# Kernel tuning notes

Hardware: AMD Instinct MI355X
Metric: run time of the kernel (lower is better)

The kernel has to match this reference:

```python
import jax, jax.numpy as jnp
import numpy as np
from jax import lax

DIM = 256
PROJ = 128
NPOS = 8          # ceil(log2(2*64+5))
EXT = 64          # attnExtension
NLAYERS = 4
HEADS = 4
KDIM = PROJ + NPOS
EPS = 1e-5


def _ln(x):
    # LayerNorm over last dim, no affine (elementwise_affine=False)
    mu = jnp.mean(x, axis=-1, keepdims=True)
    var = jnp.mean(jnp.square(x - mu), axis=-1, keepdims=True)
    return (x - mu) * lax.rsqrt(var + EPS)


def setup_inputs() -> dict:
    key = jax.random.key(0)
    ks = jax.random.split(key, 18)
    L = 2048
    s = 0.05
    return {
        "input": jax.random.normal(ks[0], (L, PROJ), jnp.float32),
        "residual": jax.random.normal(ks[1], (5 * L, DIM), jnp.float32),
        "W_proj": jax.random.normal(ks[2], (5 * DIM, KDIM), jnp.float32) * s,
        "b_proj": jnp.zeros((5 * DIM,), jnp.float32),
        "Wq": jax.random.normal(ks[3], (DIM, DIM), jnp.float32) * s,
        "bq": jnp.zeros((DIM,), jnp.float32),
        "Wk": jax.random.normal(ks[4], (DIM, KDIM), jnp.float32) * s,
        "bk": jnp.zeros((DIM,), jnp.float32),
        "Wv": jax.random.normal(ks[5], (DIM, KDIM), jnp.float32) * s,
        "bv": jnp.zeros((DIM,), jnp.float32),
        "Wo": jax.random.normal(ks[6], (DIM, DIM), jnp.float32) * s,
        "bo": jnp.zeros((DIM,), jnp.float32),
        "conv_w": jax.random.normal(ks[7], (NLAYERS, DIM, DIM, 3), jnp.float32) * s,
        "conv_b": jnp.zeros((NLAYERS, DIM), jnp.float32),
        "W_skip": jax.random.normal(ks[8], (DIM, DIM), jnp.float32) * s,
        "b_skip": jnp.zeros((DIM,), jnp.float32),
    }


def reference(input, residual, W_proj, b_proj, Wq, bq, Wk, bk, Wv, bv,
              Wo, bo, conv_w, conv_b, W_skip, b_skip):
    L = input.shape[0]
    T = 5 * L  # tgt length
    hd = DIM // HEADS

    # positional embeddings: pos[:, i] = (arange(L) % 2^(i+1)) / 2^i
    n = jnp.arange(L, dtype=input.dtype)[:, None]
    i = jnp.arange(NPOS, dtype=input.dtype)[None, :]
    pos = jnp.mod(n, 2.0 ** (i + 1.0)) / (2.0 ** i)

    src = jnp.concatenate([input, pos], axis=1)            # (L, KDIM)
    tgt = (src @ W_proj.T + b_proj).reshape(T, DIM)        # (5L, DIM)

    # banded mask: row j may attend col i iff 5i-EXT <= j < 5i+5+EXT
    j = jnp.arange(T)[:, None]
    ii = jnp.arange(L)[None, :]
    d = j - 5 * ii
    allowed = (d >= -EXT) & (d < 5 + EXT)                  # (5L, L)

    # multihead attention (eval mode, dropout skipped)
    q = (tgt @ Wq.T + bq).reshape(T, HEADS, hd).transpose(1, 0, 2)
    k = (src @ Wk.T + bk).reshape(L, HEADS, hd).transpose(1, 0, 2)
    v = (src @ Wv.T + bv).reshape(L, HEADS, hd).transpose(1, 0, 2)
    scores = jnp.einsum('hqd,hkd->hqk', q, k) / jnp.sqrt(jnp.asarray(hd, q.dtype))
    scores = jnp.where(allowed[None], scores, -jnp.inf)
    attn = jax.nn.softmax(scores, axis=-1)
    ctx = jnp.einsum('hqk,hkd->hqd', attn, v).transpose(1, 0, 2).reshape(T, DIM)
    attn_out = ctx @ Wo.T + bo

    cnn_in = _ln(attn_out) + residual                      # (5L, DIM)

    # spectral-norm conv stack (weights assumed pre-normalized) + tanh
    x = cnn_in.T[None]                                     # (1, DIM, 5L)
    for l in range(NLAYERS):
        x = jnp.tanh(
            lax.conv_general_dilated(x, conv_w[l], window_strides=(1,),
                                     padding=[(1, 1)])
            + conv_b[l][None, :, None])
    cnn_out = x[0].T                                       # (5L, DIM)

    return _ln(cnn_out + cnn_in @ W_skip.T + b_skip)
```

## Files before the change

### kernel.cpp

```cpp
#include <hip/hip_runtime.h>
#include <hip/hip_bf16.h>

#define PROJ 128
#define KPAD 192
#define EPS 1e-5f

typedef __attribute__((ext_vector_type(4))) float f32x4;
typedef __attribute__((ext_vector_type(8))) short bf16x8;
typedef __attribute__((ext_vector_type(4))) unsigned int u32x4;

__device__ inline float bflo(unsigned u){ union{unsigned x;float f;}c; c.x = u<<16; return c.f; }
__device__ inline float bfhi(unsigned u){ union{unsigned x;float f;}c; c.x = u & 0xffff0000u; return c.f; }
__device__ inline float bf2f(unsigned short u){ union{unsigned x;float f;}c; c.x = ((unsigned)u)<<16; return c.f; }
__device__ inline unsigned short f2bf(float f){
    union{float f; unsigned u;} c; c.f = f;
    unsigned r = c.u + 0x7fff + ((c.u >> 16) & 1);
    return (unsigned short)(r >> 16);
}
__device__ __forceinline__ bf16x8 asbf(u32x4 u){ union{u32x4 a; bf16x8 b;} c; c.a = u; return c.b; }

__global__ __launch_bounds__(256) void prep_all(
    const float* __restrict__ W_proj, const float* __restrict__ Wq,
    const float* __restrict__ Wk, const float* __restrict__ Wv,
    const float* __restrict__ Wo, const float* __restrict__ Ws,
    const float* __restrict__ convw, const float* __restrict__ input,
    const float* __restrict__ bq, const float* __restrict__ b_proj,
    unsigned short* __restrict__ Wqb, unsigned short* __restrict__ Wkb,
    unsigned short* __restrict__ Wvb, unsigned short* __restrict__ Wob,
    unsigned short* __restrict__ Wsb, unsigned short* __restrict__ Wcb,
    unsigned short* __restrict__ WpbT, unsigned short* __restrict__ srcb,
    unsigned short* __restrict__ cinp, float* __restrict__ zbias,
    float* __restrict__ bqc, int L, int T)
{
    int idx = blockIdx.x * 256 + threadIdx.x;
    if (idx < 65536) { Wqb[idx] = f2bf(Wq[idx]); return; }
    idx -= 65536;
    if (idx < 49152) {
        int r = idx / 192, c = idx % 192;
        Wkb[idx] = (c < 136) ? f2bf(Wk[(size_t)r * 136 + c]) : (unsigned short)0;
        return;
    }
    idx -= 49152;
    if (idx < 49152) {
        int r = idx / 192, c = idx % 192;
        Wvb[idx] = (c < 136) ? f2bf(Wv[(size_t)r * 136 + c]) : (unsigned short)0;
        return;
    }
    idx -= 49152;
    if (idx < 65536) { Wob[idx] = f2bf(Wo[idx]); return; }
    idx -= 65536;
    if (idx < 65536) {
        int e = idx & 7;
        int lane = (idx >> 3) & 63;
        int fr = (idx >> 9) & 3;
        int wid = (idx >> 11) & 7;
        int kt = idx >> 14;
        int j = fr >> 1, ks = fr & 1;
        int kq = lane >> 4, rowf = lane & 15;
        int o = wid * 32 + j * 16 + rowf;
        int c = kt * 64 + ks * 32 + kq * 8 + e;
        Wsb[idx] = f2bf(Ws[(size_t)o * 256 + c]);
        return;
    }
    idx -= 65536;
    if (idx < 786432) {
        int e = idx & 7;
        int lane = (idx >> 3) & 63;
        int fr = (idx >> 9) & 3;
        int wid = (idx >> 11) & 7;
        int ktl = idx >> 14;
        int l = ktl / 12, kt = ktl % 12;
        int j = fr >> 1, ks = fr & 1;
        int kq = lane >> 4, rowf = lane & 15;
        int o = wid * 32 + j * 16 + rowf;
        int c = kt * 64 + ks * 32 + kq * 8 + e;
        int ktap = c >> 8, ci = c & 255;
        Wcb[idx] = f2bf(convw[(((size_t)l * 256 + o) * 256 + ci) * 3 + ktap]);
        return;
    }
    idx -= 786432;
    if (idx < 327680) {
        int r = idx >> 16;
        int rem = idx & 65535;
        int c = rem >> 8, d = rem & 255;
        WpbT[idx] = (c < 136) ? f2bf(W_proj[(size_t)(r * 256 + d) * 136 + c])
                              : (unsigned short)0;
        return;
    }
    idx -= 327680;
    if (idx < L * KPAD) {
        int n = idx / KPAD, c = idx % KPAD;
        float v = 0.f;
        if (c < PROJ) v = input[(size_t)n * PROJ + c];
        else if (c < PROJ + 8) {
            int i = c - PROJ;
            int mask = (2 << i) - 1;
            v = (float)(n & mask) / (float)(1 << i);
        }
        srcb[idx] = f2bf(v);
        return;
    }
    idx -= L * KPAD;
    if (idx < 512) {
        int row = idx >> 8, c = idx & 255;
        size_t o = (row == 0) ? (size_t)c : (size_t)(T + 1) * 256 + c;
        cinp[o] = 0;
        return;
    }
    idx -= 512;
    if (idx < 256) { zbias[idx] = 0.f; return; }
    idx -= 256;
    if (idx < 1280) {
        int r = idx >> 8, o = idx & 255;
        float s = bq[o];
        const float* wrow = Wq + (size_t)o * 256;
        const float* bp = b_proj + r * 256;
        for (int c = 0; c < 256; ++c) s += wrow[c] * bp[c];
        bqc[idx] = s;
    }
}

__device__ __forceinline__ void gemm_core_64x128(
    unsigned short (&As)[64][72], unsigned short (&Bs)[128][72],
    const unsigned short* __restrict__ A, int lda,
    const unsigned short* __restrict__ B, int ldb,
    const float* __restrict__ bias,
    unsigned short* __restrict__ C, int ldc,
    int K, int m0, int n0)
{
    const int tid = threadIdx.x;
    const int lane = tid & 63;
    const int wid = tid >> 6;
    const int wm = wid >> 1, wn = wid & 1;

    const int ar = tid >> 2, asg = tid & 3;
    const int br = tid >> 1, bsg = tid & 1;

    const unsigned short* Ap = A + (size_t)(m0 + ar) * lda + asg * 16;
    const unsigned short* Bp = B + (size_t)(n0 + br) * ldb + bsg * 32;

    u32x4 ra0, ra1, rb0, rb1, rb2, rb3;
    auto loadregs = [&](int k0) {
        ra0 = *(const u32x4*)(Ap + k0);
        ra1 = *(const u32x4*)(Ap + k0 + 8);
        rb0 = *(const u32x4*)(Bp + k0);
        rb1 = *(const u32x4*)(Bp + k0 + 8);
        rb2 = *(const u32x4*)(Bp + k0 + 16);
        rb3 = *(const u32x4*)(Bp + k0 + 24);
    };
    auto stlds = [&]() {
        *(u32x4*)&As[ar][asg * 16]      = ra0;
        *(u32x4*)&As[ar][asg * 16 + 8]  = ra1;
        *(u32x4*)&Bs[br][bsg * 32]      = rb0;
        *(u32x4*)&Bs[br][bsg * 32 + 8]  = rb1;
        *(u32x4*)&Bs[br][bsg * 32 + 16] = rb2;
        *(u32x4*)&Bs[br][bsg * 32 + 24] = rb3;
    };

    f32x4 acc[2][4];
    #pragma unroll
    for (int i = 0; i < 2; ++i)
        #pragma unroll
        for (int j = 0; j < 4; ++j) acc[i][j] = (f32x4){0.f, 0.f, 0.f, 0.f};

    loadregs(0);
    stlds();
    __syncthreads();

    const int rowf = lane & 15, kb = lane >> 4;
    const int ktiles = K >> 6;
    for (int kt = 0; kt < ktiles; ++kt) {
        if (kt + 1 < ktiles) loadregs((kt + 1) << 6);
        #pragma unroll
        for (int ks = 0; ks < 2; ++ks) {
            bf16x8 af[2], bfr[4];
            #pragma unroll
            for (int i = 0; i < 2; ++i)
                af[i] = *(const bf16x8*)&As[wm * 32 + i * 16 + rowf][ks * 32 + kb * 8];
            #pragma unroll
            for (int j = 0; j < 4; ++j)
                bfr[j] = *(const bf16x8*)&Bs[wn * 64 + j * 16 + rowf][ks * 32 + kb * 8];
            #pragma unroll
            for (int i = 0; i < 2; ++i)
                #pragma unroll
                for (int j = 0; j < 4; ++j)
                    acc[i][j] = __builtin_amdgcn_mfma_f32_16x16x32_bf16(af[i], bfr[j], acc[i][j], 0, 0, 0);
        }
        __syncthreads();
        if (kt + 1 < ktiles) { stlds(); __syncthreads(); }
    }

    const int rq = lane >> 4;
    #pragma unroll
    for (int i = 0; i < 2; ++i) {
        int gm = m0 + wm * 32 + i * 16 + rq * 4;
        #pragma unroll
        for (int j = 0; j < 4; ++j) {
            int gn = n0 + wn * 64 + j * 16 + rowf;
            float bv = bias[gn];
            #pragma unroll
            for (int r = 0; r < 4; ++r)
                C[(size_t)(gm + r) * ldc + gn] = f2bf(acc[i][j][r] + bv);
        }
    }
}

__global__ __launch_bounds__(256) void combine_wq(
    const unsigned short* __restrict__ Wqb,
    const unsigned short* __restrict__ WpbT,
    const float* __restrict__ zbias,
    unsigned short* __restrict__ Wqpb)
{
    __shared__ unsigned short As[64][72];
    __shared__ unsigned short Bs[128][72];
    int bi = blockIdx.x;
    int r = bi >> 3, rem = bi & 7;
    int m0 = (rem >> 1) * 64, n0 = (rem & 1) * 128;
    gemm_core_64x128(As, Bs, Wqb, 256, WpbT + (size_t)r * 65536, 256, zbias,
                     Wqpb + (size_t)r * 65536, 256, 256, m0, n0);
}

__global__ __launch_bounds__(256) void qkv_fused(
    const unsigned short* __restrict__ srcb,
    const unsigned short* __restrict__ Wqpb,
    const unsigned short* __restrict__ Wkb,
    const unsigned short* __restrict__ Wvb,
    const float* __restrict__ bqc, const float* __restrict__ bk,
    const float* __restrict__ bv,
    unsigned short* __restrict__ qb, unsigned short* __restrict__ kb,
    unsigned short* __restrict__ vb)
{
    __shared__ unsigned short As[64][72];
    __shared__ unsigned short Bs[128][72];
    int bi = blockIdx.x;
    const unsigned short *B;
    const float* bias;
    unsigned short* C;
    int ldb, K, m0, n0, ldc;
    if (bi < 320) {
        B = Wqpb; bias = bqc; C = qb; ldb = 256; K = 192; ldc = 1280;
        m0 = (bi / 10) * 64; n0 = (bi % 10) * 128;
    } else if (bi < 384) {
        int t = bi - 320;
        B = Wkb; bias = bk; C = kb; ldb = 192; K = 192; ldc = 256;
        m0 = (t >> 1) * 64; n0 = (t & 1) * 128;
    } else {
        int t = bi - 384;
        B = Wvb; bias = bv; C = vb; ldb = 192; K = 192; ldc = 256;
        m0 = (t >> 1) * 64; n0 = (t & 1) * 128;
    }
    gemm_core_64x128(As, Bs, srcb, KPAD, B, ldb, bias, C, ldc, K, m0, n0);
}

__global__ __launch_bounds__(512) void gemm_ln0(
    const unsigned short* __restrict__ A, int lda,
    const unsigned short* __restrict__ B,
    const float* __restrict__ bias,
    const float* __restrict__ residual,
    unsigned short* __restrict__ out_bf)
{
    __shared__ unsigned short As[64][72];
    __shared__ unsigned short Bs[256][72];
    __shared__ float redS[64][4];
    __shared__ float redQ[64][4];

    const int tid = threadIdx.x;
    const int lane = tid & 63;
    const int wid = tid >> 6;
    const int wm = wid >> 2, wn = wid & 3;
    const int m0 = blockIdx.x * 64;

    const int arow = tid >> 3, acol = (tid & 7) * 8;
    const int brow = tid >> 1, bcol = (tid & 1) * 32;
    const unsigned short* Ap = A + (size_t)(m0 + arow) * lda + acol;
    const unsigned short* Bp = B + (size_t)brow * 256 + bcol;

    u32x4 ra, rb0, rb1, rb2, rb3;
    auto loadregs = [&](int k0) {
        ra  = *(const u32x4*)(Ap + k0);
        rb0 = *(const u32x4*)(Bp + k0);
        rb1 = *(const u32x4*)(Bp + k0 + 8);
        rb2 = *(const u32x4*)(Bp + k0 + 16);
        rb3 = *(const u32x4*)(Bp + k0 + 24);
    };
    auto stlds = [&]() {
        *(u32x4*)&As[arow][acol]       = ra;
        *(u32x4*)&Bs[brow][bcol]       = rb0;
        *(u32x4*)&Bs[brow][bcol + 8]   = rb1;
        *(u32x4*)&Bs[brow][bcol + 16]  = rb2;
        *(u32x4*)&Bs[brow][bcol + 24]  = rb3;
    };

    f32x4 acc[2][4];
    #pragma unroll
    for (int i = 0; i < 2; ++i)
        #pragma unroll
        for (int j = 0; j < 4; ++j) acc[i][j] = (f32x4){0.f, 0.f, 0.f, 0.f};

    loadregs(0);
    stlds();
    __syncthreads();

    const int rowf = lane & 15, kb = lane >> 4;
    #pragma unroll
    for (int kt = 0; kt < 4; ++kt) {
        if (kt < 3) loadregs((kt + 1) << 6);
        #pragma unroll
        for (int ks = 0; ks < 2; ++ks) {
            bf16x8 af[2], bfr[4];
            #pragma unroll
            for (int i = 0; i < 2; ++i)
                af[i] = *(const bf16x8*)&As[wm * 32 + i * 16 + rowf][ks * 32 + kb * 8];
            #pragma unroll
            for (int j = 0; j < 4; ++j)
                bfr[j] = *(const bf16x8*)&Bs[wn * 64 + j * 16 + rowf][ks * 32 + kb * 8];
            #pragma unroll
            for (int i = 0; i < 2; ++i)
                #pragma unroll
                for (int j = 0; j < 4; ++j)
                    acc[i][j] = __builtin_amdgcn_mfma_f32_16x16x32_bf16(af[i], bfr[j], acc[i][j], 0, 0, 0);
        }
        __syncthreads();
        if (kt < 3) { stlds(); __syncthreads(); }
    }

    const int rq = lane >> 4;
    float val[2][4][4];
    #pragma unroll
    for (int i = 0; i < 2; ++i)
        #pragma unroll
        for (int j = 0; j < 4; ++j) {
            int gn = wn * 64 + j * 16 + rowf;
            float bv = bias[gn];
            #pragma unroll
            for (int r = 0; r < 4; ++r) val[i][j][r] = acc[i][j][r] + bv;
        }

    #pragma unroll
    for (int i = 0; i < 2; ++i)
        #pragma unroll
        for (int r = 0; r < 4; ++r) {
            float s = val[i][0][r] + val[i][1][r] + val[i][2][r] + val[i][3][r];
            float q = val[i][0][r] * val[i][0][r] + val[i][1][r] * val[i][1][r]
                    + val[i][2][r] * val[i][2][r] + val[i][3][r] * val[i][3][r];
            #pragma unroll
            for (int m = 1; m < 16; m <<= 1) {
                s += __shfl_xor(s, m, 64);
                q += __shfl_xor(q, m, 64);
            }
            if (rowf == 0) {
                int row = wm * 32 + i * 16 + rq * 4 + r;
                redS[row][wn] = s;
                redQ[row][wn] = q;
            }
        }
    __syncthreads();

    #pragma unroll
    for (int i = 0; i < 2; ++i) {
        #pragma unroll
        for (int r = 0; r < 4; ++r) {
            int row = wm * 32 + i * 16 + rq * 4 + r;
            int gm = m0 + row;
            float s = redS[row][0] + redS[row][1] + redS[row][2] + redS[row][3];
            float q = redQ[row][0] + redQ[row][1] + redQ[row][2] + redQ[row][3];
            float mu = s * (1.f / 256.f);
            float var = q * (1.f / 256.f) - mu * mu;
            float rs = rsqrtf(var + EPS);
            #pragma unroll
            for (int j = 0; j < 4; ++j) {
                int gn = wn * 64 + j * 16 + rowf;
                float nv = (val[i][j][r] - mu) * rs + residual[(size_t)gm * 256 + gn];
                out_bf[(size_t)(gm + 1) * 256 + gn] = f2bf(nv);
            }
        }
    }
}

__global__ __launch_bounds__(256) void attn16(
    const unsigned short* __restrict__ q,
    const unsigned short* __restrict__ k,
    const unsigned short* __restrict__ v,
    unsigned short* __restrict__ ctx, int L)
{
    __shared__ unsigned short ksm[30][264];
    __shared__ unsigned short vsm[30][264];
    const int j0 = blockIdx.x * 16;
    const int iblk0 = (j0 >= 68) ? (j0 - 64) / 5 : 0;
    int ihim = (j0 + 79) / 5; if (ihim > L - 1) ihim = L - 1;
    const int NR = ihim - iblk0 + 1;

    for (int e = threadIdx.x; e < 30 * 32; e += 256) {
        int rr = e >> 5, cc = (e & 31) * 8;
        u32x4 kz = {0, 0, 0, 0}, vz = {0, 0, 0, 0};
        if (rr < NR) {
            kz = *(const u32x4*)&k[(size_t)(iblk0 + rr) * 256 + cc];
            vz = *(const u32x4*)&v[(size_t)(iblk0 + rr) * 256 + cc];
        }
        *(u32x4*)&ksm[rr][cc] = kz;
        *(u32x4*)&vsm[rr][cc] = vz;
    }
    __syncthreads();

    const int tid = threadIdx.x;
    const int h = tid >> 6, lane = tid & 63;
    const int qq = lane & 15, p = lane >> 4;
    const int j = j0 + qq;
    const int colb = h * 64 + p * 16;

    float qr[16];
    {
        u32x4 q0 = *(const u32x4*)&q[(size_t)j * 256 + colb];
        u32x4 q1 = *(const u32x4*)&q[(size_t)j * 256 + colb + 8];
        #pragma unroll
        for (int w = 0; w < 4; ++w) {
            qr[2 * w]     = bflo(q0[w]) * 0.125f;
            qr[2 * w + 1] = bfhi(q0[w]) * 0.125f;
            qr[8 + 2 * w]     = bflo(q1[w]) * 0.125f;
            qr[8 + 2 * w + 1] = bfhi(q1[w]) * 0.125f;
        }
    }
    const int ilo = (j >= 68) ? (j - 64) / 5 : 0;
    int ihi = (j + 64) / 5; if (ihi > L - 1) ihi = L - 1;

    float sc[30];
    #pragma unroll
    for (int t = 0; t < 30; ++t) {
        int i = iblk0 + t;
        u32x4 k0 = *(const u32x4*)&ksm[t][colb];
        u32x4 k1 = *(const u32x4*)&ksm[t][colb + 8];
        float s = 0.f;
        #pragma unroll
        for (int w = 0; w < 4; ++w) {
            s += qr[2 * w]     * bflo(k0[w]);
            s += qr[2 * w + 1] * bfhi(k0[w]);
            s += qr[8 + 2 * w]     * bflo(k1[w]);
            s += qr[8 + 2 * w + 1] * bfhi(k1[w]);
        }
        s += __shfl_xor(s, 16, 64);
        s += __shfl_xor(s, 32, 64);
        sc[t] = (i >= ilo && i <= ihi) ? s : -1e30f;
    }
    float mx = -1e30f;
    #pragma unroll
    for (int t = 0; t < 30; ++t) mx = fmaxf(mx, sc[t]);
    float den = 0.f, o[16];
    #pragma unroll
    for (int d = 0; d < 16; ++d) o[d] = 0.f;
    #pragma unroll
    for (int t = 0; t < 30; ++t) {
        float pt = __expf(sc[t] - mx);
        den += pt;
        u32x4 v0 = *(const u32x4*)&vsm[t][colb];
        u32x4 v1 = *(const u32x4*)&vsm[t][colb + 8];
        #pragma unroll
        for (int w = 0; w < 4; ++w) {
            o[2 * w]     += pt * bflo(v0[w]);
            o[2 * w + 1] += pt * bfhi(v0[w]);
            o[8 + 2 * w]     += pt * bflo(v1[w]);
            o[8 + 2 * w + 1] += pt * bfhi(v1[w]);
        }
    }
    float inv = 1.f / den;
    #pragma unroll
    for (int d = 0; d < 16; ++d)
        ctx[(size_t)j * 256 + colb + d] = f2bf(o[d] * inv);
}

#define CVALID 40
template<int NKT, bool ISCONV>
__device__ __forceinline__ void frag_gemm(
    const unsigned short* __restrict__ Wp,
    unsigned short (*actin)[264],
    f32x4 (&acc)[3][2], int wid, int lane)
{
    const int rowf = lane & 15, kq = lane >> 4;
    const unsigned short* base = Wp + wid * 2048 + lane * 8;
    u32x4 A0, A1, A2, A3, B0, B1, B2, B3;

    asm volatile(
        "global_load_dwordx4 %0, %4, off\n\t"
        "global_load_dwordx4 %1, %4, off offset:1024\n\t"
        "global_load_dwordx4 %2, %4, off offset:2048\n\t"
        "global_load_dwordx4 %3, %4, off offset:3072"
        : "=&v"(A0), "=&v"(A1), "=&v"(A2), "=&v"(A3)
        : "v"(base));
    asm volatile("s_waitcnt vmcnt(0)"
                 : "+v"(A0), "+v"(A1), "+v"(A2), "+v"(A3));

    auto body = [&](int kt, u32x4& c0, u32x4& c1, u32x4& c2, u32x4& c3,
                            u32x4& n0, u32x4& n1, u32x4& n2, u32x4& n3) {
        if (kt + 1 < NKT) {
            const unsigned short* nb = base + (size_t)(kt + 1) * 16384;
            asm volatile(
                "global_load_dwordx4 %0, %4, off\n\t"
                "global_load_dwordx4 %1, %4, off offset:1024\n\t"
                "global_load_dwordx4 %2, %4, off offset:2048\n\t"
                "global_load_dwordx4 %3, %4, off offset:3072"
                : "=&v"(n0), "=&v"(n1), "=&v"(n2), "=&v"(n3)
                : "v"(nb));
        }
        const int dt = ISCONV ? (kt >> 2) : 1;
        const int cb = ISCONV ? ((kt & 3) * 64) : (kt * 64);
        #pragma unroll
        for (int ks = 0; ks < 2; ++ks) {
            bf16x8 a0 = *(const bf16x8*)&actin[rowf + dt][cb + ks * 32 + kq * 8];
            bf16x8 a1 = *(const bf16x8*)&actin[16 + rowf + dt][cb + ks * 32 + kq * 8];
            bf16x8 a2 = *(const bf16x8*)&actin[32 + rowf + dt][cb + ks * 32 + kq * 8];
            bf16x8 w0 = asbf(ks ? c1 : c0);
            bf16x8 w1 = asbf(ks ? c3 : c2);
            acc[0][0] = __builtin_amdgcn_mfma_f32_16x16x32_bf16(a0, w0, acc[0][0], 0, 0, 0);
            acc[0][1] = __builtin_amdgcn_mfma_f32_16x16x32_bf16(a0, w1, acc[0][1], 0, 0, 0);
            acc[1][0] = __builtin_amdgcn_mfma_f32_16x16x32_bf16(a1, w0, acc[1][0], 0, 0, 0);
            acc[1][1] = __builtin_amdgcn_mfma_f32_16x16x32_bf16(a1, w1, acc[1][1], 0, 0, 0);
            acc[2][0] = __builtin_amdgcn_mfma_f32_16x16x32_bf16(a2, w0, acc[2][0], 0, 0, 0);
            acc[2][1] = __builtin_amdgcn_mfma_f32_16x16x32_bf16(a2, w1, acc[2][1], 0, 0, 0);
        }
        if (kt + 1 < NKT)
            asm volatile("s_waitcnt vmcnt(0)"
                         : "+v"(n0), "+v"(n1), "+v"(n2), "+v"(n3));
    };

    #pragma unroll
    for (int k2 = 0; k2 < NKT; k2 += 2) {
        body(k2,     A0, A1, A2, A3, B0, B1, B2, B3);
        body(k2 + 1, B0, B1, B2, B3, A0, A1, A2, A3);
    }
}

__global__ __launch_bounds__(512)
__attribute__((amdgpu_waves_per_eu(2)))
void conv_skip_ln(
    const unsigned short* __restrict__ cinp,
    const unsigned short* __restrict__ Wcb,
    const float* __restrict__ conv_b,
    const unsigned short* __restrict__ Wsb,
    const float* __restrict__ b_skip,
    float* __restrict__ out, int T)
{
    __shared__ unsigned short actA[50][264];
    __shared__ unsigned short actB[50][264];
    __shared__ float redS[48][8];
    __shared__ float redQ[48][8];

    const int tid = threadIdx.x;
    const int lane = tid & 63;
    const int wid = tid >> 6;
    const int rowf = lane & 15;
    const int kq = lane >> 4;
    const int t0 = blockIdx.x * CVALID;

    for (int e = tid; e < 50 * 32; e += 512) {
        int b = e >> 5, c = (e & 31) * 8;
        int g = t0 - 5 + b;
        u32x4 z = {0, 0, 0, 0};
        if (g >= -1 && g <= T)
            z = *(const u32x4*)&cinp[(size_t)(g + 1) * 256 + c];
        *(u32x4*)&actA[b][c] = z;
    }
    if (tid < 256) actB[0][tid] = 0; else actB[49][tid - 256] = 0;
    __syncthreads();

    f32x4 skipacc[3][2];
    #pragma unroll
    for (int i = 0; i < 3; ++i)
        #pragma unroll
        for (int j = 0; j < 2; ++j) skipacc[i][j] = (f32x4){0.f, 0.f, 0.f, 0.f};
    frag_gemm<4, false>(Wsb, actA, skipacc, wid, lane);

    const int gn0 = wid * 32 + rowf;
    f32x4 cacc[3][2];
    #pragma unroll 1
    for (int l = 0; l < 4; ++l) {
        #pragma unroll
        for (int i = 0; i < 3; ++i)
            #pragma unroll
            for (int j = 0; j < 2; ++j) cacc[i][j] = (f32x4){0.f, 0.f, 0.f, 0.f};
        unsigned short (*ain)[264]  = (l & 1) ? actB : actA;
        unsigned short (*aout)[264] = (l & 1) ? actA : actB;
        frag_gemm<12, true>(Wcb + (size_t)l * 196608, ain, cacc, wid, lane);

        float b0 = conv_b[l * 256 + gn0];
        float b1 = conv_b[l * 256 + gn0 + 16];
        if (l < 3) {
            #pragma unroll
            for (int i = 0; i < 3; ++i)
                #pragma unroll
                for (int r = 0; r < 4; ++r) {
                    int w = i * 16 + kq * 4 + r;
                    int g = t0 - 4 + w;
                    bool ok = (g >= 0 && g < T);
                    float v0 = cacc[i][0][r] + b0;
                    float v1 = cacc[i][1][r] + b1;
                    v0 = 1.f - 2.f / (__expf(2.f * v0) + 1.f);
                    v1 = 1.f - 2.f / (__expf(2.f * v1) + 1.f);
                    aout[w + 1][gn0]      = ok ? f2bf(v0) : (unsigned short)0;
                    aout[w + 1][gn0 + 16] = ok ? f2bf(v1) : (unsigned short)0;
                }
            if (tid < 256) aout[0][tid] = 0; else aout[49][tid - 256] = 0;
            __syncthreads();
        } else {
            float sb0 = b_skip[gn0], sb1 = b_skip[gn0 + 16];
            #pragma unroll
            for (int i = 0; i < 3; ++i)
                #pragma unroll
                for (int r = 0; r < 4; ++r) {
                    int w = i * 16 + kq * 4 + r;
                    int g = t0 - 4 + w;
                    bool ok = (g >= 0 && g < T);
                    float v0 = cacc[i][0][r] + b0;
                    float v1 = cacc[i][1][r] + b1;
                    v0 = ok ? (1.f - 2.f / (__expf(2.f * v0) + 1.f)) : 0.f;
                    v1 = ok ? (1.f - 2.f / (__expf(2.f * v1) + 1.f)) : 0.f;
                    skipacc[i][0][r] += sb0 + v0;
                    skipacc[i][1][r] += sb1 + v1;
                }
        }
    }

    #pragma unroll
    for (int i = 0; i < 3; ++i)
        #pragma unroll
        for (int r = 0; r < 4; ++r) {
            float a = skipacc[i][0][r], b = skipacc[i][1][r];
            float s = a + b;
            float q = a * a + b * b;
            #pragma unroll
            for (int m = 1; m < 16; m <<= 1) {
                s += __shfl_xor(s, m, 64);
                q += __shfl_xor(q, m, 64);
            }
            if (rowf == 0) {
                int row = i * 16 + kq * 4 + r;
                redS[row][wid] = s;
                redQ[row][wid] = q;
            }
        }
    __syncthreads();

    #pragma unroll
    for (int i = 0; i < 3; ++i)
        #pragma unroll
        for (int r = 0; r < 4; ++r) {
            int row = i * 16 + kq * 4 + r;
            if (row < 4 || row >= 44) continue;
            int g = t0 - 4 + row;
            if (g >= T) continue;
            float s = 0.f, q = 0.f;
            #pragma unroll
            for (int x = 0; x < 8; ++x) { s += redS[row][x]; q += redQ[row][x]; }
            float mu = s * (1.f / 256.f);
            float var = q * (1.f / 256.f) - mu * mu;
            float rs = rsqrtf(var + EPS);
            out[(size_t)g * 256 + gn0]      = (skipacc[i][0][r] - mu) * rs;
            out[(size_t)g * 256 + gn0 + 16] = (skipacc[i][1][r] - mu) * rs;
        }
}

extern "C" void kernel_launch(void* const* d_in, const int* in_sizes, int n_in,
                              void* d_out, int out_size, void* d_ws, size_t ws_size,
                              hipStream_t stream) {
    const float* input    = (const float*)d_in[0];
    const float* residual = (const float*)d_in[1];
    const float* W_proj   = (const float*)d_in[2];
    const float* b_proj   = (const float*)d_in[3];
    const float* Wq       = (const float*)d_in[4];
    const float* bq       = (const float*)d_in[5];
    const float* Wk       = (const float*)d_in[6];
    const float* bk       = (const float*)d_in[7];
    const float* Wv       = (const float*)d_in[8];
    const float* bv       = (const float*)d_in[9];
    const float* Wo       = (const float*)d_in[10];
    const float* bo       = (const float*)d_in[11];
    const float* conv_w   = (const float*)d_in[12];
    const float* conv_b   = (const float*)d_in[13];
    const float* W_skip   = (const float*)d_in[14];
    const float* b_skip   = (const float*)d_in[15];
    float* out = (float*)d_out;

    const int L = in_sizes[0] / PROJ;
    const int T = 5 * L;

    unsigned short* w16 = (unsigned short*)d_ws;
    size_t off = 0;
    auto alloc = [&](size_t n) { unsigned short* p = w16 + off; off += n; return p; };
    unsigned short* Wqb   = alloc(65536);
    unsigned short* Wkb   = alloc(49152);
    unsigned short* Wvb   = alloc(49152);
    unsigned short* Wob   = alloc(65536);
    unsigned short* Wsb   = alloc(65536);
    unsigned short* Wcb   = alloc(786432);
    unsigned short* WpbT  = alloc(327680);
    unsigned short* Wqpb  = alloc(327680);
    unsigned short* srcb  = alloc((size_t)L * KPAD);
    unsigned short* tgtb  = alloc((size_t)T * 256);
    unsigned short* qb    = alloc((size_t)T * 256);
    unsigned short* kb    = alloc((size_t)L * 256);
    unsigned short* vb    = alloc((size_t)L * 256);
    unsigned short* cinp  = alloc((size_t)(T + 2) * 256);
    float* zbias = (float*)alloc(512);
    float* bqc   = (float*)alloc(2560);

    prep_all<<<dim3(7048), 256, 0, stream>>>(
        W_proj, Wq, Wk, Wv, Wo, W_skip, conv_w, input, bq, b_proj,
        Wqb, Wkb, Wvb, Wob, Wsb, Wcb, WpbT, srcb, cinp, zbias, bqc, L, T);

    combine_wq<<<dim3(40), 256, 0, stream>>>(Wqb, WpbT, zbias, Wqpb);

    qkv_fused<<<dim3(448), 256, 0, stream>>>(
        srcb, Wqpb, Wkb, Wvb, bqc, bk, bv, qb, kb, vb);

    attn16<<<dim3(T / 16), 256, 0, stream>>>(qb, kb, vb, tgtb, L);

    gemm_ln0<<<dim3(T / 64), 512, 0, stream>>>(tgtb, 256, Wob, bo, residual, cinp);

    conv_skip_ln<<<dim3(T / CVALID), 512, 0, stream>>>(
        cinp, Wcb, conv_b, Wsb, b_skip, out, T);
}
```

Before: 100.00 us.

## Deepen weight prefetch to two stages and parallelize bias fold with wave reductions

The frag_gemm weight loads now keep two k-tiles in flight. The next-next tile is issued right after the MFMAs, and a vmcnt(4) wait only covers the older tile, so global load latency overlaps more compute. Separately, the bq+Wq·b_proj bias fold in prep_all moves from a serial 256-iteration loop per thread to one wavefront per output with a shuffle reduction, placed first so it no longer forms a long tail. The cost is more in-flight registers and a larger prep grid.

```diff
diff --git a/kernel.cpp b/kernel.cpp
--- a/kernel.cpp
+++ b/kernel.cpp
@@ -33,6 +33,20 @@
     float* __restrict__ bqc, int L, int T)
 {
     int idx = blockIdx.x * 256 + threadIdx.x;
+    if (idx < 81920) {
+        int w = idx >> 6, lanei = idx & 63;
+        int r = w >> 8, o = w & 255;
+        const float* wrow = Wq + (size_t)o * 256;
+        const float* bp = b_proj + r * 256;
+        float s = 0.f;
+        #pragma unroll
+        for (int c = 0; c < 256; c += 64) s += wrow[c + lanei] * bp[c + lanei];
+        #pragma unroll
+        for (int m = 32; m > 0; m >>= 1) s += __shfl_xor(s, m, 64);
+        if (lanei == 0) bqc[w] = s + bq[o];
+        return;
+    }
+    idx -= 81920;
     if (idx < 65536) { Wqb[idx] = f2bf(Wq[idx]); return; }
     idx -= 65536;
     if (idx < 49152) {
@@ -109,15 +123,6 @@
     }
     idx -= 512;
     if (idx < 256) { zbias[idx] = 0.f; return; }
-    idx -= 256;
-    if (idx < 1280) {
-        int r = idx >> 8, o = idx & 255;
-        float s = bq[o];
-        const float* wrow = Wq + (size_t)o * 256;
-        const float* bp = b_proj + r * 256;
-        for (int c = 0; c < 256; ++c) s += wrow[c] * bp[c];
-        bqc[idx] = s;
-    }
 }
 
 __device__ __forceinline__ void gemm_core_64x128(
@@ -468,6 +473,24 @@
 }
 
 #define CVALID 40
+
+__device__ __forceinline__ void wload4(u32x4& r0, u32x4& r1, u32x4& r2, u32x4& r3,
+                                       const unsigned short* p) {
+    asm volatile(
+        "global_load_dwordx4 %0, %4, off\n\t"
+        "global_load_dwordx4 %1, %4, off offset:1024\n\t"
+        "global_load_dwordx4 %2, %4, off offset:2048\n\t"
+        "global_load_dwordx4 %3, %4, off offset:3072"
+        : "=&v"(r0), "=&v"(r1), "=&v"(r2), "=&v"(r3)
+        : "v"(p));
+}
+__device__ __forceinline__ void wwait4(u32x4& r0, u32x4& r1, u32x4& r2, u32x4& r3) {
+    asm volatile("s_waitcnt vmcnt(4)" : "+v"(r0), "+v"(r1), "+v"(r2), "+v"(r3));
+}
+__device__ __forceinline__ void wwait0(u32x4& r0, u32x4& r1, u32x4& r2, u32x4& r3) {
+    asm volatile("s_waitcnt vmcnt(0)" : "+v"(r0), "+v"(r1), "+v"(r2), "+v"(r3));
+}
+
 template<int NKT, bool ISCONV>
 __device__ __forceinline__ void frag_gemm(
     const unsigned short* __restrict__ Wp,
@@ -478,28 +501,16 @@
     const unsigned short* base = Wp + wid * 2048 + lane * 8;
     u32x4 A0, A1, A2, A3, B0, B1, B2, B3;
 
-    asm volatile(
-        "global_load_dwordx4 %0, %4, off\n\t"
-        "global_load_dwordx4 %1, %4, off offset:1024\n\t"
-        "global_load_dwordx4 %2, %4, off offset:2048\n\t"
-        "global_load_dwordx4 %3, %4, off offset:3072"
-        : "=&v"(A0), "=&v"(A1), "=&v"(A2), "=&v"(A3)
-        : "v"(base));
-    asm volatile("s_waitcnt vmcnt(0)"
-                 : "+v"(A0), "+v"(A1), "+v"(A2), "+v"(A3));
+    wload4(A0, A1, A2, A3, base);
+    if (NKT > 1) {
+        wload4(B0, B1, B2, B3, base + 16384);
+        wwait4(A0, A1, A2, A3);
+    } else {
+        wwait0(A0, A1, A2, A3);
+    }
 
     auto body = [&](int kt, u32x4& c0, u32x4& c1, u32x4& c2, u32x4& c3,
                             u32x4& n0, u32x4& n1, u32x4& n2, u32x4& n3) {
-        if (kt + 1 < NKT) {
-            const unsigned short* nb = base + (size_t)(kt + 1) * 16384;
-            asm volatile(
-                "global_load_dwordx4 %0, %4, off\n\t"
-                "global_load_dwordx4 %1, %4, off offset:1024\n\t"
-                "global_load_dwordx4 %2, %4, off offset:2048\n\t"
-                "global_load_dwordx4 %3, %4, off offset:3072"
-                : "=&v"(n0), "=&v"(n1), "=&v"(n2), "=&v"(n3)
-                : "v"(nb));
-        }
         const int dt = ISCONV ? (kt >> 2) : 1;
         const int cb = ISCONV ? ((kt & 3) * 64) : (kt * 64);
         #pragma unroll
@@ -516,9 +527,12 @@
             acc[2][0] = __builtin_amdgcn_mfma_f32_16x16x32_bf16(a2, w0, acc[2][0], 0, 0, 0);
             acc[2][1] = __builtin_amdgcn_mfma_f32_16x16x32_bf16(a2, w1, acc[2][1], 0, 0, 0);
         }
-        if (kt + 1 < NKT)
-            asm volatile("s_waitcnt vmcnt(0)"
-                         : "+v"(n0), "+v"(n1), "+v"(n2), "+v"(n3));
+        if (kt + 2 < NKT) {
+            wload4(c0, c1, c2, c3, base + (size_t)(kt + 2) * 16384);
+            wwait4(n0, n1, n2, n3);
+        } else if (kt + 1 < NKT) {
+            wwait0(n0, n1, n2, n3);
+        }
     };
 
     #pragma unroll
@@ -701,7 +715,7 @@
     float* zbias = (float*)alloc(512);
     float* bqc   = (float*)alloc(2560);
 
-    prep_all<<<dim3(7048), 256, 0, stream>>>(
+    prep_all<<<dim3(7363), 256, 0, stream>>>(
         W_proj, Wq, Wk, Wv, Wo, W_skip, conv_w, input, bq, b_proj,
         Wqb, Wkb, Wvb, Wob, Wsb, Wcb, WpbT, srcb, cinp, zbias, bqc, L, T);
 
```

New measurement: 88.17 us. 11.8% less time.
